# Optimization experiments

Measured on AMD Instinct MI355X. Metric: run time of the kernel, lower is better.

The kernel has to match this reference:

```python
import jax, jax.numpy as jnp
import numpy as np

# Grid parameters (from init_kwargs)
GRID_W, GRID_L, GRID_H = 96, 96, 48
VOXEL_SIZE = 0.05
MIN_POINTS_PER_VOXEL = 10


def setup_inputs() -> dict:
    key = jax.random.key(0)
    k1, k2 = jax.random.split(key, 2)
    # points uniform over a ~[0,1.5]^3 sub-volume so voxel occupancy is realistic
    point_coordinates = jax.random.uniform(k1, (4, 3, 480, 640), jnp.float32) * 1.5
    point_attributes = jax.random.normal(k2, (4, 16, 480, 640), jnp.float32)
    origin = jnp.zeros((4, 3), jnp.float32)
    return {"point_coordinates": point_coordinates,
            "point_attributes": point_attributes,
            "origin": origin}


def _voxelize_one(coords, attrs, org):
    # coords: [3, N], attrs: [C, N], org: [3]
    V = GRID_W * GRID_L * GRID_H
    bounds = jnp.array([GRID_W, GRID_L, GRID_H], jnp.int32)
    # per-point voxel index (floor == .long() for positive; OOB handled by mask)
    idx3 = jnp.floor((coords - org[:, None]) / VOXEL_SIZE).astype(jnp.int32)  # [3, N]
    in_bounds = jnp.all((idx3 >= 0) & (idx3 < bounds[:, None]), axis=0)       # [N]
    flat = idx3[0] * (GRID_L * GRID_H) + idx3[1] * GRID_H + idx3[2]           # [N]
    flat = jnp.where(in_bounds, flat, 0)  # route OOB points to voxel 0, masked out
    # occupancy: scatter-add of in-bounds mask
    counts = jax.ops.segment_sum(in_bounds.astype(jnp.float32), flat, num_segments=V)
    # max-pool of attributes per voxel; OOB points contribute -inf
    masked = jnp.where(in_bounds[None, :], attrs, -jnp.inf)                   # [C, N]
    vmax = jax.ops.segment_max(masked.T, flat, num_segments=V).T              # [C, V]
    occ = counts >= MIN_POINTS_PER_VOXEL                                      # [V]
    data = jnp.where(occ[None, :] & jnp.isfinite(vmax), vmax, 0.0)            # [C, V]
    return data, occ


def reference(point_coordinates, point_attributes, origin):
    b, c = point_attributes.shape[:2]
    coords = point_coordinates.reshape(b, 3, -1)   # [B, 3, N]
    attrs = point_attributes.reshape(b, c, -1)     # [B, C, N]
    data, occ = jax.vmap(_voxelize_one)(coords, attrs, origin)
    voxeldata = data.reshape(b, c, GRID_W, GRID_L, GRID_H)
    voxeloccupancy = occ.reshape(b, 1, GRID_W, GRID_L, GRID_H).astype(jnp.float32)
    return voxeldata, voxeloccupancy
```

## Files before the change

kernel.cpp:

```cpp
#include <hip/hip_runtime.h>
#include <cstdint>
#include <math.h>

#define GRID_W 96
#define GRID_L 96
#define GRID_H 48
#define NVOX (GRID_W * GRID_L * GRID_H)
#define VOXEL_SIZE 0.05f
#define MIN_PTS 10
#define BATCH 4
#define CHANS 16
#define NPTS (480 * 640)
#define TOTPTS (BATCH * NPTS)
#define TOTVOX (BATCH * NVOX)

#define SCAN_BLKS 864
#define SCAN_TPB 256
#define SCAN_EPT 8
#define SCAN_CHUNK (SCAN_TPB * SCAN_EPT)

#define ROWW 8

typedef unsigned nt_uint4  __attribute__((ext_vector_type(4)));
typedef float    nt_float4 __attribute__((ext_vector_type(4)));
typedef float    nt_float2 __attribute__((ext_vector_type(2)));

#define WS_OFFSETS 0
#define WS_VR      ((TOTVOX + 4) * 4)
#define WS_IDS     (WS_VR + TOTPTS * 4)
#define WS_ROWS    (WS_IDS + TOTPTS * 4 + 16)
#define WS_SUMS    (WS_ROWS + (size_t)TOTPTS * ROWW * 4)
#define WS_NEEDED  ((size_t)(WS_SUMS + 4096))

__device__ __forceinline__ unsigned bf16_rtne(float f) {
    unsigned u = __float_as_uint(f);
    return (u + 0x7FFFu + ((u >> 16) & 1u)) >> 16;
}
__device__ __forceinline__ unsigned pack2(float lo, float hi) {
    return bf16_rtne(lo) | (bf16_rtne(hi) << 16);
}


__global__ void k_hist_pack(const float* __restrict__ coords,
                            const float* __restrict__ attrs,
                            const float* __restrict__ origin,
                            unsigned*    __restrict__ vr,
                            unsigned*    __restrict__ rows,
                            unsigned*    __restrict__ cnt)
{
    int t = blockIdx.x * blockDim.x + threadIdx.x;
    if (t >= TOTPTS / 2) return;
    int pid = t * 2;
    int b = pid / NPTS;
    int n = pid - b * NPTS;

    const float* cb = coords + (size_t)b * 3 * NPTS;
    nt_float2 X = __builtin_nontemporal_load((const nt_float2*)(cb + n));
    nt_float2 Y = __builtin_nontemporal_load((const nt_float2*)(cb + NPTS + n));
    nt_float2 Z = __builtin_nontemporal_load((const nt_float2*)(cb + 2 * NPTS + n));
    float ox = origin[b * 3 + 0];
    float oy = origin[b * 3 + 1];
    float oz = origin[b * 3 + 2];

    const float* ab = attrs + (size_t)b * CHANS * NPTS + n;
    unsigned w[2][ROWW];
    #pragma unroll
    for (int c = 0; c < CHANS; c += 2) {
        nt_float2 a0 = __builtin_nontemporal_load((const nt_float2*)(ab + (size_t)c * NPTS));
        nt_float2 a1 = __builtin_nontemporal_load((const nt_float2*)(ab + (size_t)(c + 1) * NPTS));
        w[0][c >> 1] = pack2(a0.x, a1.x);
        w[1][c >> 1] = pack2(a0.y, a1.y);
    }
    uint4* dst = (uint4*)(rows + (size_t)pid * ROWW);
    dst[0] = uint4{w[0][0], w[0][1], w[0][2], w[0][3]};
    dst[1] = uint4{w[0][4], w[0][5], w[0][6], w[0][7]};
    dst[2] = uint4{w[1][0], w[1][1], w[1][2], w[1][3]};
    dst[3] = uint4{w[1][4], w[1][5], w[1][6], w[1][7]};

    float xs[2] = {X.x, X.y};
    float ys[2] = {Y.x, Y.y};
    float zs[2] = {Z.x, Z.y};
    unsigned ps[2];
    #pragma unroll
    for (int k = 0; k < 2; ++k) {
        int ix = (int)floorf((xs[k] - ox) / VOXEL_SIZE);
        int iy = (int)floorf((ys[k] - oy) / VOXEL_SIZE);
        int iz = (int)floorf((zs[k] - oz) / VOXEL_SIZE);
        unsigned p = 0xFFFFFFFFu;
        if ((unsigned)ix < GRID_W && (unsigned)iy < GRID_L && (unsigned)iz < GRID_H) {
            int v = b * NVOX + ix * (GRID_L * GRID_H) + iy * GRID_H + iz;
            unsigned r = atomicAdd(&cnt[v], 1u);
            p = ((unsigned)v << 10) | (r & 1023u);
        }
        ps[k] = p;
    }
    *(uint2*)(vr + pid) = uint2{ps[0], ps[1]};
}

__global__ void k_scan1(unsigned* __restrict__ offsets,
                        unsigned* __restrict__ sums,
                        float*    __restrict__ occ)
{
    __shared__ unsigned s[SCAN_TPB];
    int t = threadIdx.x;
    int base = blockIdx.x * SCAN_CHUNK + t * SCAN_EPT;

    uint4 a = ((const uint4*)(offsets + base))[0];
    uint4 c = ((const uint4*)(offsets + base))[1];
    unsigned e[SCAN_EPT] = {a.x, a.y, a.z, a.w, c.x, c.y, c.z, c.w};

    nt_float4 oc0, oc1;
    oc0.x = (e[0] >= MIN_PTS) ? 1.f : 0.f;  oc0.y = (e[1] >= MIN_PTS) ? 1.f : 0.f;
    oc0.z = (e[2] >= MIN_PTS) ? 1.f : 0.f;  oc0.w = (e[3] >= MIN_PTS) ? 1.f : 0.f;
    oc1.x = (e[4] >= MIN_PTS) ? 1.f : 0.f;  oc1.y = (e[5] >= MIN_PTS) ? 1.f : 0.f;
    oc1.z = (e[6] >= MIN_PTS) ? 1.f : 0.f;  oc1.w = (e[7] >= MIN_PTS) ? 1.f : 0.f;
    __builtin_nontemporal_store(oc0, ((nt_float4*)(occ + base)));
    __builtin_nontemporal_store(oc1, ((nt_float4*)(occ + base)) + 1);

    unsigned tot = 0;
    #pragma unroll
    for (int k = 0; k < SCAN_EPT; ++k) { unsigned v = e[k]; e[k] = tot; tot += v; }

    s[t] = tot;
    __syncthreads();
    #pragma unroll
    for (int off = 1; off < SCAN_TPB; off <<= 1) {
        unsigned v = (t >= off) ? s[t - off] : 0u;
        __syncthreads();
        s[t] += v;
        __syncthreads();
    }
    unsigned prefix = s[t] - tot;
    #pragma unroll
    for (int k = 0; k < SCAN_EPT; ++k) e[k] += prefix;

    ((uint4*)(offsets + base))[0] = uint4{e[0], e[1], e[2], e[3]};
    ((uint4*)(offsets + base))[1] = uint4{e[4], e[5], e[6], e[7]};

    if (t == SCAN_TPB - 1) sums[blockIdx.x] = s[t];
}

__global__ void k_scan2(unsigned* __restrict__ sums) {
    __shared__ unsigned s[1024];
    int t = threadIdx.x;
    unsigned my = (t < SCAN_BLKS) ? sums[t] : 0u;
    s[t] = my;
    __syncthreads();
    #pragma unroll
    for (int off = 1; off < 1024; off <<= 1) {
        unsigned v = (t >= off) ? s[t - off] : 0u;
        __syncthreads();
        s[t] += v;
        __syncthreads();
    }
    if (t < SCAN_BLKS) sums[t] = s[t] - my;
    if (t == SCAN_BLKS - 1) sums[SCAN_BLKS] = s[t];
}

__global__ void k_scatter_ids4(const unsigned* __restrict__ vr,
                               const unsigned* __restrict__ offsets,
                               const unsigned* __restrict__ sums,
                               int*            __restrict__ ids)
{
    int t = blockIdx.x * blockDim.x + threadIdx.x;
    if (t >= TOTPTS / 4) return;
    int pid = t * 4;
    uint4 P = *(const uint4*)(vr + pid);
    unsigned ps[4] = {P.x, P.y, P.z, P.w};
    #pragma unroll
    for (int k = 0; k < 4; ++k) {
        if (ps[k] != 0xFFFFFFFFu) {
            unsigned v = ps[k] >> 10;
            unsigned pos = offsets[v] + sums[v >> 11] + (ps[k] & 1023u);
            ids[pos] = pid + k;
        }
    }
}

__global__ void k_gather_ind2(const unsigned* __restrict__ rows,
                              const int*      __restrict__ ids,
                              const unsigned* __restrict__ offsets,
                              const unsigned* __restrict__ sums,
                              float*          __restrict__ data)
{
    int g = blockIdx.x * blockDim.x + threadIdx.x;
    if (g >= TOTVOX / 2) return;
    int vox0 = g * 2;

    uint2 O = *(const uint2*)(offsets + vox0);
    unsigned base = sums[vox0 >> 11];
    unsigned s[3];
    s[0] = O.x + base;
    s[1] = O.y + base;
    s[2] = offsets[vox0 + 2] + sums[(vox0 + 2) >> 11];

    float m[2][CHANS];
    #pragma unroll
    for (int q = 0; q < 2; ++q) {
        unsigned k = s[q + 1] - s[q];
        unsigned s0 = s[q];
        if (k >= MIN_PTS) {
            const float ninf = -__builtin_inff();
            #pragma unroll
            for (int c = 0; c < CHANS; ++c) m[q][c] = ninf;
            unsigned j = 0;
            for (; j + 2 <= k; j += 2) {
                int p0 = ids[s0 + j];
                int p1 = ids[s0 + j + 1];
                const uint4* r0p = (const uint4*)(rows + (size_t)p0 * ROWW);
                const uint4* r1p = (const uint4*)(rows + (size_t)p1 * ROWW);
                uint4 l0 = r0p[0], h0 = r0p[1];
                uint4 l1 = r1p[0], h1 = r1p[1];
                unsigned wa[8] = {l0.x, l0.y, l0.z, l0.w, h0.x, h0.y, h0.z, h0.w};
                unsigned wb[8] = {l1.x, l1.y, l1.z, l1.w, h1.x, h1.y, h1.z, h1.w};
                #pragma unroll
                for (int h = 0; h < 8; ++h) {
                    m[q][2 * h]     = fmaxf(m[q][2 * h],
                                        fmaxf(__uint_as_float(wa[h] << 16),
                                              __uint_as_float(wb[h] << 16)));
                    m[q][2 * h + 1] = fmaxf(m[q][2 * h + 1],
                                        fmaxf(__uint_as_float(wa[h] & 0xFFFF0000u),
                                              __uint_as_float(wb[h] & 0xFFFF0000u)));
                }
            }
            if (j < k) {
                int p0 = ids[s0 + j];
                const uint4* r0p = (const uint4*)(rows + (size_t)p0 * ROWW);
                uint4 l0 = r0p[0], h0 = r0p[1];
                unsigned wa[8] = {l0.x, l0.y, l0.z, l0.w, h0.x, h0.y, h0.z, h0.w};
                #pragma unroll
                for (int h = 0; h < 8; ++h) {
                    m[q][2 * h]     = fmaxf(m[q][2 * h], __uint_as_float(wa[h] << 16));
                    m[q][2 * h + 1] = fmaxf(m[q][2 * h + 1],
                                            __uint_as_float(wa[h] & 0xFFFF0000u));
                }
            }
            #pragma unroll
            for (int c = 0; c < CHANS; ++c) if (!isfinite(m[q][c])) m[q][c] = 0.f;
        } else {
            #pragma unroll
            for (int c = 0; c < CHANS; ++c) m[q][c] = 0.f;
        }
    }

    int b = vox0 / NVOX;
    int v0 = vox0 - b * NVOX;
    float* db = data + (size_t)b * CHANS * NVOX + v0;
    #pragma unroll
    for (int c = 0; c < CHANS; ++c) {
        nt_float2 o = {m[0][c], m[1][c]};
        __builtin_nontemporal_store(o, (nt_float2*)(db + (size_t)c * NVOX));
    }
}


__device__ __forceinline__ unsigned flip_f32(float f) {
    unsigned u = __float_as_uint(f);
    unsigned mask = (unsigned)(-(int)(u >> 31)) | 0x80000000u;
    return u ^ mask;
}
__device__ __forceinline__ float unflip_f32(unsigned u) {
    unsigned mask = ((u >> 31) - 1u) | 0x80000000u;
    return __uint_as_float(u ^ mask);
}
#define FLIP_NEG_INF 0x007FFFFFu

__global__ void pv_init(uint4* __restrict__ out) {
    const int DATA4 = BATCH * CHANS * NVOX / 4;
    const int TOT4  = BATCH * (CHANS + 1) * NVOX / 4;
    int i = blockIdx.x * blockDim.x + threadIdx.x;
    if (i < TOT4) {
        unsigned val = (i < DATA4) ? FLIP_NEG_INF : 0u;
        out[i] = uint4{val, val, val, val};
    }
}

__global__ void pv_scatter(const float* __restrict__ coords,
                           const float* __restrict__ attrs,
                           const float* __restrict__ origin,
                           unsigned*    __restrict__ data_u,
                           unsigned*    __restrict__ cnt)
{
    int id = blockIdx.x * blockDim.x + threadIdx.x;
    if (id >= TOTPTS) return;
    int b = id / NPTS;
    int n = id - b * NPTS;
    const float* cb = coords + (size_t)b * 3 * NPTS;
    float x = cb[n], y = cb[NPTS + n], z = cb[2 * NPTS + n];
    float ox = origin[b * 3 + 0], oy = origin[b * 3 + 1], oz = origin[b * 3 + 2];
    int ix = (int)floorf((x - ox) / VOXEL_SIZE);
    int iy = (int)floorf((y - oy) / VOXEL_SIZE);
    int iz = (int)floorf((z - oz) / VOXEL_SIZE);
    if ((unsigned)ix < GRID_W && (unsigned)iy < GRID_L && (unsigned)iz < GRID_H) {
        int flat = ix * (GRID_L * GRID_H) + iy * GRID_H + iz;
        atomicAdd(&cnt[b * NVOX + flat], 1u);
        const float* ab = attrs + (size_t)b * CHANS * NPTS + n;
        unsigned*    db = data_u + (size_t)b * CHANS * NVOX + flat;
        #pragma unroll
        for (int c = 0; c < CHANS; ++c)
            atomicMax(&db[(size_t)c * NVOX], flip_f32(ab[(size_t)c * NPTS]));
    }
}

__global__ void pv_finalize(unsigned* __restrict__ data_u,
                            unsigned* __restrict__ cnt_u)
{
    int id = blockIdx.x * blockDim.x + threadIdx.x;
    if (id >= TOTVOX) return;
    int b = id / NVOX;
    int v = id - b * NVOX;
    unsigned cnt = cnt_u[id];
    bool occ = (cnt >= MIN_PTS);
    ((float*)cnt_u)[id] = occ ? 1.0f : 0.0f;
    unsigned* db = data_u + (size_t)b * CHANS * NVOX + v;
    #pragma unroll
    for (int c = 0; c < CHANS; ++c) {
        float f = unflip_f32(db[(size_t)c * NVOX]);
        ((float*)db)[(size_t)c * NVOX] = (occ && isfinite(f)) ? f : 0.0f;
    }
}


extern "C" void kernel_launch(void* const* d_in, const int* in_sizes, int n_in,
                              void* d_out, int out_size, void* d_ws, size_t ws_size,
                              hipStream_t stream) {
    const float* coords = (const float*)d_in[0];
    const float* attrs  = (const float*)d_in[1];
    const float* origin = (const float*)d_in[2];

    float* out = (float*)d_out;
    float* data = out;
    float* occ  = out + (size_t)BATCH * CHANS * NVOX;

    if (ws_size >= WS_NEEDED) {
        char* ws = (char*)d_ws;
        unsigned* offsets = (unsigned*)(ws + WS_OFFSETS);
        unsigned* vr      = (unsigned*)(ws + WS_VR);
        int*      ids     = (int*)(ws + WS_IDS);
        unsigned* rows    = (unsigned*)(ws + WS_ROWS);
        unsigned* sums    = (unsigned*)(ws + WS_SUMS);

        (void)hipMemsetAsync(offsets, 0, (size_t)(TOTVOX + 4) * 4, stream);
        k_hist_pack<<<(TOTPTS / 2 + 255) / 256, 256, 0, stream>>>(coords, attrs, origin,
                                                                  vr, rows, offsets);
        k_scan1<<<SCAN_BLKS, SCAN_TPB, 0, stream>>>(offsets, sums, occ);
        k_scan2<<<1, 1024, 0, stream>>>(sums);
        k_scatter_ids4<<<(TOTPTS / 4 + 255) / 256, 256, 0, stream>>>(vr, offsets, sums, ids);
        k_gather_ind2<<<(TOTVOX / 2 + 255) / 256, 256, 0, stream>>>(rows, ids, offsets, sums, data);
    } else {
        unsigned* data_u = (unsigned*)data;
        unsigned* cnt    = (unsigned*)occ;
        const int TOT4 = BATCH * (CHANS + 1) * NVOX / 4;
        pv_init<<<(TOT4 + 255) / 256, 256, 0, stream>>>((uint4*)d_out);
        pv_scatter<<<(TOTPTS + 255) / 256, 256, 0, stream>>>(coords, attrs, origin, data_u, cnt);
        pv_finalize<<<(TOTVOX + 255) / 256, 256, 0, stream>>>(data_u, cnt);
    }
}
```

Measured before the change: 287.4 us.

## Privatize voxel histogram per XCD with packed 16-bit counters

```diff
diff --git a/kernel.cpp b/kernel.cpp
--- a/kernel.cpp
+++ b/kernel.cpp
@@ -13,6 +13,7 @@
 #define NPTS (480 * 640)
 #define TOTPTS (BATCH * NPTS)
 #define TOTVOX (BATCH * NVOX)
+#define HALFVOX (TOTVOX / 2)
 
 #define SCAN_BLKS 864
 #define SCAN_TPB 256
@@ -20,13 +21,15 @@
 #define SCAN_CHUNK (SCAN_TPB * SCAN_EPT)
 
 #define ROWW 8
+#define NXCD 8
 
 typedef unsigned nt_uint4  __attribute__((ext_vector_type(4)));
 typedef float    nt_float4 __attribute__((ext_vector_type(4)));
 typedef float    nt_float2 __attribute__((ext_vector_type(2)));
 
 #define WS_OFFSETS 0
-#define WS_VR      ((TOTVOX + 4) * 4)
+#define WS_CNT8    ((TOTVOX + 4) * 4)
+#define WS_VR      (WS_CNT8 + NXCD * HALFVOX * 4)
 #define WS_IDS     (WS_VR + TOTPTS * 4)
 #define WS_ROWS    (WS_IDS + TOTPTS * 4 + 16)
 #define WS_SUMS    (WS_ROWS + (size_t)TOTPTS * ROWW * 4)
@@ -46,7 +49,7 @@
                             const float* __restrict__ origin,
                             unsigned*    __restrict__ vr,
                             unsigned*    __restrict__ rows,
-                            unsigned*    __restrict__ cnt)
+                            unsigned*    __restrict__ cnt8)
 {
     int t = blockIdx.x * blockDim.x + threadIdx.x;
     if (t >= TOTPTS / 2) return;
@@ -77,6 +80,11 @@
     dst[2] = uint4{w[1][0], w[1][1], w[1][2], w[1][3]};
     dst[3] = uint4{w[1][4], w[1][5], w[1][6], w[1][7]};
 
+    unsigned xcc;
+    asm volatile("s_getreg_b32 %0, hwreg(HW_REG_XCC_ID, 0, 32)" : "=s"(xcc));
+    xcc &= (NXCD - 1);
+    unsigned* plane = cnt8 + (size_t)xcc * HALFVOX;
+
     float xs[2] = {X.x, X.y};
     float ys[2] = {Y.x, Y.y};
     float zs[2] = {Z.x, Z.y};
@@ -88,26 +96,38 @@
         int iz = (int)floorf((zs[k] - oz) / VOXEL_SIZE);
         unsigned p = 0xFFFFFFFFu;
         if ((unsigned)ix < GRID_W && (unsigned)iy < GRID_L && (unsigned)iz < GRID_H) {
-            int v = b * NVOX + ix * (GRID_L * GRID_H) + iy * GRID_H + iz;
-            unsigned r = atomicAdd(&cnt[v], 1u);
-            p = ((unsigned)v << 10) | (r & 1023u);
+            unsigned v = (unsigned)(b * NVOX + ix * (GRID_L * GRID_H) + iy * GRID_H + iz);
+            unsigned sh = (v & 1u) * 16u;
+            unsigned old = __hip_atomic_fetch_add(&plane[v >> 1], 1u << sh,
+                                                  __ATOMIC_RELAXED,
+                                                  __HIP_MEMORY_SCOPE_WORKGROUP);
+            unsigned rk = (old >> sh) & 0xFFFFu;
+            p = (v << 11) | (xcc << 8) | (rk & 255u);
         }
         ps[k] = p;
     }
     *(uint2*)(vr + pid) = uint2{ps[0], ps[1]};
 }
 
-__global__ void k_scan1(unsigned* __restrict__ offsets,
-                        unsigned* __restrict__ sums,
-                        float*    __restrict__ occ)
+__global__ void k_scan1(const unsigned* __restrict__ cnt8,
+                        unsigned*       __restrict__ offsets,
+                        unsigned*       __restrict__ sums,
+                        float*          __restrict__ occ)
 {
     __shared__ unsigned s[SCAN_TPB];
     int t = threadIdx.x;
     int base = blockIdx.x * SCAN_CHUNK + t * SCAN_EPT;
 
-    uint4 a = ((const uint4*)(offsets + base))[0];
-    uint4 c = ((const uint4*)(offsets + base))[1];
-    unsigned e[SCAN_EPT] = {a.x, a.y, a.z, a.w, c.x, c.y, c.z, c.w};
+    unsigned e[SCAN_EPT] = {0, 0, 0, 0, 0, 0, 0, 0};
+    #pragma unroll
+    for (int r = 0; r < NXCD; ++r) {
+        const uint4* p = (const uint4*)(cnt8 + (size_t)r * HALFVOX + (base >> 1));
+        uint4 a = p[0];
+        e[0] += a.x & 0xFFFFu; e[1] += a.x >> 16;
+        e[2] += a.y & 0xFFFFu; e[3] += a.y >> 16;
+        e[4] += a.z & 0xFFFFu; e[5] += a.z >> 16;
+        e[6] += a.w & 0xFFFFu; e[7] += a.w >> 16;
+    }
 
     nt_float4 oc0, oc1;
     oc0.x = (e[0] >= MIN_PTS) ? 1.f : 0.f;  oc0.y = (e[1] >= MIN_PTS) ? 1.f : 0.f;
@@ -158,6 +178,7 @@
 }
 
 __global__ void k_scatter_ids4(const unsigned* __restrict__ vr,
+                               const unsigned* __restrict__ cnt8,
                                const unsigned* __restrict__ offsets,
                                const unsigned* __restrict__ sums,
                                int*            __restrict__ ids)
@@ -169,9 +190,17 @@
     unsigned ps[4] = {P.x, P.y, P.z, P.w};
     #pragma unroll
     for (int k = 0; k < 4; ++k) {
-        if (ps[k] != 0xFFFFFFFFu) {
-            unsigned v = ps[k] >> 10;
-            unsigned pos = offsets[v] + sums[v >> 11] + (ps[k] & 1023u);
+        unsigned p = ps[k];
+        if (p != 0xFFFFFFFFu) {
+            unsigned v    = p >> 11;
+            unsigned r    = (p >> 8) & (NXCD - 1);
+            unsigned rank = p & 255u;
+            unsigned sh   = (v & 1u) * 16u;
+            unsigned wi   = v >> 1;
+            unsigned sub  = 0;
+            for (unsigned r2 = 0; r2 < r; ++r2)
+                sub += (cnt8[(size_t)r2 * HALFVOX + wi] >> sh) & 0xFFFFu;
+            unsigned pos = offsets[v] + sums[v >> 11] + sub + rank;
             ids[pos] = pid + k;
         }
     }
@@ -335,18 +364,22 @@
     if (ws_size >= WS_NEEDED) {
         char* ws = (char*)d_ws;
         unsigned* offsets = (unsigned*)(ws + WS_OFFSETS);
+        unsigned* cnt8    = (unsigned*)(ws + WS_CNT8);
         unsigned* vr      = (unsigned*)(ws + WS_VR);
         int*      ids     = (int*)(ws + WS_IDS);
         unsigned* rows    = (unsigned*)(ws + WS_ROWS);
         unsigned* sums    = (unsigned*)(ws + WS_SUMS);
 
-        (void)hipMemsetAsync(offsets, 0, (size_t)(TOTVOX + 4) * 4, stream);
+        (void)hipMemsetAsync(cnt8, 0, (size_t)NXCD * HALFVOX * 4, stream);
+        (void)hipMemsetAsync(offsets + TOTVOX, 0, 16, stream);
         k_hist_pack<<<(TOTPTS / 2 + 255) / 256, 256, 0, stream>>>(coords, attrs, origin,
-                                                                  vr, rows, offsets);
-        k_scan1<<<SCAN_BLKS, SCAN_TPB, 0, stream>>>(offsets, sums, occ);
+                                                                  vr, rows, cnt8);
+        k_scan1<<<SCAN_BLKS, SCAN_TPB, 0, stream>>>(cnt8, offsets, sums, occ);
         k_scan2<<<1, 1024, 0, stream>>>(sums);
-        k_scatter_ids4<<<(TOTPTS / 4 + 255) / 256, 256, 0, stream>>>(vr, offsets, sums, ids);
-        k_gather_ind2<<<(TOTVOX / 2 + 255) / 256, 256, 0, stream>>>(rows, ids, offsets, sums, data);
+        k_scatter_ids4<<<(TOTPTS / 4 + 255) / 256, 256, 0, stream>>>(vr, cnt8, offsets,
+                                                                     sums, ids);
+        k_gather_ind2<<<(TOTVOX / 2 + 255) / 256, 256, 0, stream>>>(rows, ids, offsets,
+                                                                    sums, data);
     } else {
         unsigned* data_u = (unsigned*)data;
         unsigned* cnt    = (unsigned*)occ;
```

New measurement: 318.4 us. +10.8%, slower.

## Compact occupied voxels into a worklist and gather only those

Applied to the files above, without the earlier changes.

```diff
diff --git a/kernel.cpp b/kernel.cpp
--- a/kernel.cpp
+++ b/kernel.cpp
@@ -21,16 +21,19 @@
 
 #define ROWW 8
 
+#define WL_MAX 131072
+
 typedef unsigned nt_uint4  __attribute__((ext_vector_type(4)));
 typedef float    nt_float4 __attribute__((ext_vector_type(4)));
 typedef float    nt_float2 __attribute__((ext_vector_type(2)));
 
 #define WS_OFFSETS 0
-#define WS_VR      ((TOTVOX + 4) * 4)
+#define WS_VR      ((TOTVOX + 8) * 4)
 #define WS_IDS     (WS_VR + TOTPTS * 4)
 #define WS_ROWS    (WS_IDS + TOTPTS * 4 + 16)
 #define WS_SUMS    (WS_ROWS + (size_t)TOTPTS * ROWW * 4)
-#define WS_NEEDED  ((size_t)(WS_SUMS + 4096))
+#define WS_WL      (WS_SUMS + 4096)
+#define WS_NEEDED  ((size_t)(WS_WL + WL_MAX * 4))
 
 __device__ __forceinline__ unsigned bf16_rtne(float f) {
     unsigned u = __float_as_uint(f);
@@ -39,6 +42,7 @@
 __device__ __forceinline__ unsigned pack2(float lo, float hi) {
     return bf16_rtne(lo) | (bf16_rtne(hi) << 16);
 }
+
 
 
 __global__ void k_hist_pack(const float* __restrict__ coords,
@@ -99,9 +103,12 @@
 
 __global__ void k_scan1(unsigned* __restrict__ offsets,
                         unsigned* __restrict__ sums,
-                        float*    __restrict__ occ)
+                        float*    __restrict__ occ,
+                        unsigned* __restrict__ wl,
+                        unsigned* __restrict__ wlcnt)
 {
     __shared__ unsigned s[SCAN_TPB];
+    __shared__ unsigned bbase;
     int t = threadIdx.x;
     int base = blockIdx.x * SCAN_CHUNK + t * SCAN_EPT;
 
@@ -109,11 +116,15 @@
     uint4 c = ((const uint4*)(offsets + base))[1];
     unsigned e[SCAN_EPT] = {a.x, a.y, a.z, a.w, c.x, c.y, c.z, c.w};
 
+    unsigned amask = 0;
+    #pragma unroll
+    for (int k = 0; k < SCAN_EPT; ++k) amask |= (e[k] >= MIN_PTS) ? (1u << k) : 0u;
+
     nt_float4 oc0, oc1;
-    oc0.x = (e[0] >= MIN_PTS) ? 1.f : 0.f;  oc0.y = (e[1] >= MIN_PTS) ? 1.f : 0.f;
-    oc0.z = (e[2] >= MIN_PTS) ? 1.f : 0.f;  oc0.w = (e[3] >= MIN_PTS) ? 1.f : 0.f;
-    oc1.x = (e[4] >= MIN_PTS) ? 1.f : 0.f;  oc1.y = (e[5] >= MIN_PTS) ? 1.f : 0.f;
-    oc1.z = (e[6] >= MIN_PTS) ? 1.f : 0.f;  oc1.w = (e[7] >= MIN_PTS) ? 1.f : 0.f;
+    oc0.x = (amask & 1u)   ? 1.f : 0.f;  oc0.y = (amask & 2u)   ? 1.f : 0.f;
+    oc0.z = (amask & 4u)   ? 1.f : 0.f;  oc0.w = (amask & 8u)   ? 1.f : 0.f;
+    oc1.x = (amask & 16u)  ? 1.f : 0.f;  oc1.y = (amask & 32u)  ? 1.f : 0.f;
+    oc1.z = (amask & 64u)  ? 1.f : 0.f;  oc1.w = (amask & 128u) ? 1.f : 0.f;
     __builtin_nontemporal_store(oc0, ((nt_float4*)(occ + base)));
     __builtin_nontemporal_store(oc1, ((nt_float4*)(occ + base)) + 1);
 
@@ -138,6 +149,26 @@
     ((uint4*)(offsets + base))[1] = uint4{e[4], e[5], e[6], e[7]};
 
     if (t == SCAN_TPB - 1) sums[blockIdx.x] = s[t];
+
+    unsigned acnt = (unsigned)__popc((int)amask);
+    __syncthreads();
+    s[t] = acnt;
+    __syncthreads();
+    #pragma unroll
+    for (int off = 1; off < SCAN_TPB; off <<= 1) {
+        unsigned v = (t >= off) ? s[t - off] : 0u;
+        __syncthreads();
+        s[t] += v;
+        __syncthreads();
+    }
+    unsigned apre = s[t] - acnt;
+    if (t == SCAN_TPB - 1) bbase = atomicAdd(wlcnt, s[t]);
+    __syncthreads();
+    unsigned wpos = bbase + apre;
+    #pragma unroll
+    for (int k = 0; k < SCAN_EPT; ++k) {
+        if (amask & (1u << k)) wl[wpos++] = (unsigned)(base + k);
+    }
 }
 
 __global__ void k_scan2(unsigned* __restrict__ sums) {
@@ -177,79 +208,68 @@
     }
 }
 
-__global__ void k_gather_ind2(const unsigned* __restrict__ rows,
-                              const int*      __restrict__ ids,
-                              const unsigned* __restrict__ offsets,
-                              const unsigned* __restrict__ sums,
-                              float*          __restrict__ data)
-{
-    int g = blockIdx.x * blockDim.x + threadIdx.x;
-    if (g >= TOTVOX / 2) return;
-    int vox0 = g * 2;
-
-    uint2 O = *(const uint2*)(offsets + vox0);
-    unsigned base = sums[vox0 >> 11];
-    unsigned s[3];
-    s[0] = O.x + base;
-    s[1] = O.y + base;
-    s[2] = offsets[vox0 + 2] + sums[(vox0 + 2) >> 11];
-
-    float m[2][CHANS];
-    #pragma unroll
-    for (int q = 0; q < 2; ++q) {
-        unsigned k = s[q + 1] - s[q];
-        unsigned s0 = s[q];
-        if (k >= MIN_PTS) {
-            const float ninf = -__builtin_inff();
+__global__ void k_gather_wl(const unsigned* __restrict__ rows,
+                            const int*      __restrict__ ids,
+                            const unsigned* __restrict__ offsets,
+                            const unsigned* __restrict__ sums,
+                            const unsigned* __restrict__ wl,
+                            const unsigned* __restrict__ wlcnt,
+                            float*          __restrict__ data)
+{
+    unsigned nwl = *wlcnt;
+    for (unsigned i = blockIdx.x * blockDim.x + threadIdx.x; i < nwl;
+         i += gridDim.x * blockDim.x) {
+        unsigned v  = wl[i];
+        unsigned s0 = offsets[v] + sums[v >> 11];
+        unsigned s1 = offsets[v + 1] + sums[(v + 1) >> 11];
+        unsigned k  = s1 - s0;
+
+        const float ninf = -__builtin_inff();
+        float m[CHANS];
+        #pragma unroll
+        for (int c = 0; c < CHANS; ++c) m[c] = ninf;
+
+        unsigned j = 0;
+        for (; j + 2 <= k; j += 2) {
+            int p0 = ids[s0 + j];
+            int p1 = ids[s0 + j + 1];
+            const uint4* r0p = (const uint4*)(rows + (size_t)p0 * ROWW);
+            const uint4* r1p = (const uint4*)(rows + (size_t)p1 * ROWW);
+            uint4 l0 = r0p[0], h0 = r0p[1];
+            uint4 l1 = r1p[0], h1 = r1p[1];
+            unsigned wa[8] = {l0.x, l0.y, l0.z, l0.w, h0.x, h0.y, h0.z, h0.w};
+            unsigned wb[8] = {l1.x, l1.y, l1.z, l1.w, h1.x, h1.y, h1.z, h1.w};
             #pragma unroll
-            for (int c = 0; c < CHANS; ++c) m[q][c] = ninf;
-            unsigned j = 0;
-            for (; j + 2 <= k; j += 2) {
-                int p0 = ids[s0 + j];
-                int p1 = ids[s0 + j + 1];
-                const uint4* r0p = (const uint4*)(rows + (size_t)p0 * ROWW);
-                const uint4* r1p = (const uint4*)(rows + (size_t)p1 * ROWW);
-                uint4 l0 = r0p[0], h0 = r0p[1];
-                uint4 l1 = r1p[0], h1 = r1p[1];
-                unsigned wa[8] = {l0.x, l0.y, l0.z, l0.w, h0.x, h0.y, h0.z, h0.w};
-                unsigned wb[8] = {l1.x, l1.y, l1.z, l1.w, h1.x, h1.y, h1.z, h1.w};
-                #pragma unroll
-                for (int h = 0; h < 8; ++h) {
-                    m[q][2 * h]     = fmaxf(m[q][2 * h],
-                                        fmaxf(__uint_as_float(wa[h] << 16),
-                                              __uint_as_float(wb[h] << 16)));
-                    m[q][2 * h + 1] = fmaxf(m[q][2 * h + 1],
-                                        fmaxf(__uint_as_float(wa[h] & 0xFFFF0000u),
-                                              __uint_as_float(wb[h] & 0xFFFF0000u)));
-                }
+            for (int h = 0; h < 8; ++h) {
+                m[2 * h]     = fmaxf(m[2 * h],
+                                 fmaxf(__uint_as_float(wa[h] << 16),
+                                       __uint_as_float(wb[h] << 16)));
+                m[2 * h + 1] = fmaxf(m[2 * h + 1],
+                                 fmaxf(__uint_as_float(wa[h] & 0xFFFF0000u),
+                                       __uint_as_float(wb[h] & 0xFFFF0000u)));
             }
-            if (j < k) {
-                int p0 = ids[s0 + j];
-                const uint4* r0p = (const uint4*)(rows + (size_t)p0 * ROWW);
-                uint4 l0 = r0p[0], h0 = r0p[1];
-                unsigned wa[8] = {l0.x, l0.y, l0.z, l0.w, h0.x, h0.y, h0.z, h0.w};
-                #pragma unroll
-                for (int h = 0; h < 8; ++h) {
-                    m[q][2 * h]     = fmaxf(m[q][2 * h], __uint_as_float(wa[h] << 16));
-                    m[q][2 * h + 1] = fmaxf(m[q][2 * h + 1],
-                                            __uint_as_float(wa[h] & 0xFFFF0000u));
-                }
+        }
+        if (j < k) {
+            int p0 = ids[s0 + j];
+            const uint4* r0p = (const uint4*)(rows + (size_t)p0 * ROWW);
+            uint4 l0 = r0p[0], h0 = r0p[1];
+            unsigned wa[8] = {l0.x, l0.y, l0.z, l0.w, h0.x, h0.y, h0.z, h0.w};
+            #pragma unroll
+            for (int h = 0; h < 8; ++h) {
+                m[2 * h]     = fmaxf(m[2 * h], __uint_as_float(wa[h] << 16));
+                m[2 * h + 1] = fmaxf(m[2 * h + 1],
+                                     __uint_as_float(wa[h] & 0xFFFF0000u));
             }
-            #pragma unroll
-            for (int c = 0; c < CHANS; ++c) if (!isfinite(m[q][c])) m[q][c] = 0.f;
-        } else {
-            #pragma unroll
-            for (int c = 0; c < CHANS; ++c) m[q][c] = 0.f;
-        }
-    }
-
-    int b = vox0 / NVOX;
-    int v0 = vox0 - b * NVOX;
-    float* db = data + (size_t)b * CHANS * NVOX + v0;
-    #pragma unroll
-    for (int c = 0; c < CHANS; ++c) {
-        nt_float2 o = {m[0][c], m[1][c]};
-        __builtin_nontemporal_store(o, (nt_float2*)(db + (size_t)c * NVOX));
+        }
+
+        unsigned b  = v / NVOX;
+        unsigned v0 = v - b * NVOX;
+        float* db = data + (size_t)b * CHANS * NVOX + v0;
+        #pragma unroll
+        for (int c = 0; c < CHANS; ++c) {
+            float f = m[c];
+            db[(size_t)c * NVOX] = isfinite(f) ? f : 0.f;
+        }
     }
 }
 
@@ -335,18 +355,21 @@
     if (ws_size >= WS_NEEDED) {
         char* ws = (char*)d_ws;
         unsigned* offsets = (unsigned*)(ws + WS_OFFSETS);
+        unsigned* wlcnt   = offsets + TOTVOX + 4;
         unsigned* vr      = (unsigned*)(ws + WS_VR);
         int*      ids     = (int*)(ws + WS_IDS);
         unsigned* rows    = (unsigned*)(ws + WS_ROWS);
         unsigned* sums    = (unsigned*)(ws + WS_SUMS);
-
-        (void)hipMemsetAsync(offsets, 0, (size_t)(TOTVOX + 4) * 4, stream);
+        unsigned* wl      = (unsigned*)(ws + WS_WL);
+
+        (void)hipMemsetAsync(offsets, 0, (size_t)(TOTVOX + 8) * 4, stream);
+        (void)hipMemsetAsync(data, 0, (size_t)BATCH * CHANS * NVOX * 4, stream);
         k_hist_pack<<<(TOTPTS / 2 + 255) / 256, 256, 0, stream>>>(coords, attrs, origin,
                                                                   vr, rows, offsets);
-        k_scan1<<<SCAN_BLKS, SCAN_TPB, 0, stream>>>(offsets, sums, occ);
+        k_scan1<<<SCAN_BLKS, SCAN_TPB, 0, stream>>>(offsets, sums, occ, wl, wlcnt);
         k_scan2<<<1, 1024, 0, stream>>>(sums);
         k_scatter_ids4<<<(TOTPTS / 4 + 255) / 256, 256, 0, stream>>>(vr, offsets, sums, ids);
-        k_gather_ind2<<<(TOTVOX / 2 + 255) / 256, 256, 0, stream>>>(rows, ids, offsets, sums, data);
+        k_gather_wl<<<512, 256, 0, stream>>>(rows, ids, offsets, sums, wl, wlcnt, data);
     } else {
         unsigned* data_u = (unsigned*)data;
         unsigned* cnt    = (unsigned*)occ;
```

Result: slower. 310.3 us (+8.0%).
